# Performance work log

Measured on AMD Instinct MI355X. Metric: run time of the kernel, lower is better.

## Reference

```python
import jax, jax.numpy as jnp
import numpy as np
import math

B, C, H, W = 8, 96, 128, 128


def cos_map(N):
    wx = (jnp.arange(N, dtype=jnp.float32) + 0.5) / N          # [N]
    wn = jnp.arange(N, dtype=jnp.float32)[:, None]             # [N,1]
    w = jnp.cos(wn * wx[None, :] * jnp.pi) * math.sqrt(2.0 / N)
    return w.at[0, :].multiply(1.0 / math.sqrt(2.0))            # [N,N] (n, x)


def decay_map(h, w):
    wn = jnp.linspace(0.0, jnp.pi, h + 1)[:h][:, None]
    wm = jnp.linspace(0.0, jnp.pi, w + 1)[:w][None, :]
    return jnp.exp(-(wn ** 2 + wm ** 2))                        # [h,w]


def setup_inputs() -> dict:
    key = jax.random.key(0)
    ks = jax.random.split(key, 20)
    s = 0.02
    return {
        'x': jax.random.normal(ks[0], (B, C, H, W), jnp.float32),
        'freq_embed': jax.random.normal(ks[1], (H, W, C), jnp.float32),
        'outline_feat': jax.random.normal(ks[2], (B, H, W, C), jnp.float32),
        'dw_w': jax.random.normal(ks[3], (C, 1, 3, 3), jnp.float32) * s,
        'dw_b': jnp.zeros((C,), jnp.float32),
        'lin_w': jax.random.normal(ks[4], (2 * C, C), jnp.float32) * s,
        'lin_b': jnp.zeros((2 * C,), jnp.float32),
        'k_w': jax.random.normal(ks[5], (C, C), jnp.float32) * s,
        'k_b': jnp.zeros((C,), jnp.float32),
        'lin2_w': jax.random.normal(ks[6], (2 * C, 2 * C), jnp.float32) * s,
        'lin2_b': jnp.zeros((2 * C,), jnp.float32),
        'k2_w': jax.random.normal(ks[7], (2 * C, 2 * C), jnp.float32) * s,
        'k2_b': jnp.zeros((2 * C,), jnp.float32),
        'lin3_w': jax.random.normal(ks[8], (C, 2 * C), jnp.float32) * s,
        'lin3_b': jnp.zeros((C,), jnp.float32),
        'ln_g': jnp.ones((C,), jnp.float32),
        'ln_b': jnp.zeros((C,), jnp.float32),
        'out_w': jax.random.normal(ks[9], (C, C), jnp.float32) * s,
        'out_b': jnp.zeros((C,), jnp.float32),
    }


def dct2(u, cn, cm):
    # u: [B,H,W,C] -> [B,N,M,C]
    u = jnp.einsum('nh,bhwc->bnwc', cn, u)
    return jnp.einsum('mw,bnwc->bnmc', cm, u)


def idct2(u, cn, cm):
    # u: [B,N,M,C] -> [B,H,W,C]
    u = jnp.einsum('nh,bnmc->bhmc', cn, u)
    return jnp.einsum('mw,bhmc->bhwc', cm, u)


def layernorm(u, g, b, eps=1e-5):
    mu = jnp.mean(u, axis=-1, keepdims=True)
    var = jnp.var(u, axis=-1, keepdims=True)
    return (u - mu) * jax.lax.rsqrt(var + eps) * g + b


def reference(x, freq_embed, outline_feat, dw_w, dw_b, lin_w, lin_b, k_w, k_b,
              lin2_w, lin2_b, k2_w, k2_b, lin3_w, lin3_b, ln_g, ln_b, out_w, out_b):
    # depthwise 3x3 conv, padding 1 (NCHW)
    x = jax.lax.conv_general_dilated(
        x, dw_w, window_strides=(1, 1), padding=((1, 1), (1, 1)),
        dimension_numbers=('NCHW', 'OIHW', 'NCHW'), feature_group_count=C)
    x = x + dw_b[None, :, None, None]
    x = jnp.transpose(x, (0, 2, 3, 1))                          # [B,H,W,C]
    h = jnp.einsum('bhwc,dc->bhwd', x, lin_w) + lin_b           # [B,H,W,2C]
    x, z = jnp.split(h, 2, axis=-1)

    cn, cm = cos_map(H), cos_map(W)
    dec = decay_map(H, W)                                       # [H,W]

    # first heat pass
    x = dct2(x, cn, cm)                                         # [B,N,M,C]
    otfeat = jnp.mean(outline_feat, axis=0)                     # [H,W,C]
    k = jax.nn.relu(jnp.einsum('hwc,dc->hwd', freq_embed + otfeat, k_w) + k_b)
    x = x * jnp.power(dec[:, :, None], k)                       # [B,N,M,C]
    x = idct2(x, cn, cm)                                        # [B,H,W,C]

    # second heat pass on concatenated features
    x = jnp.concatenate([x, outline_feat], axis=-1)             # [B,H,W,2C]
    skfeat = jnp.mean(jnp.einsum('bhwc,dc->bhwd', x, lin2_w) + lin2_b, axis=0)  # [H,W,2C]
    x = dct2(x, cn, cm)
    k2 = jax.nn.relu(jnp.einsum('hwc,dc->hwd', skfeat, k2_w) + k2_b)
    x = x * jnp.power(dec[:, :, None], k2)
    x = idct2(x, cn, cm)                                        # [B,H,W,2C]

    x = jnp.einsum('bhwc,dc->bhwd', x, lin3_w) + lin3_b         # [B,H,W,C]
    x = layernorm(x, ln_g, ln_b)
    x = x * jax.nn.silu(z)
    x = jnp.einsum('bhwc,dc->bhwd', x, out_w) + out_b
    return jnp.transpose(x, (0, 3, 1, 2))                       # [B,C,H,W]
```

## Files before the change

### kernel.cpp

```cpp
#include <hip/hip_runtime.h>
#include <math.h>
#include <stdint.h>

#ifndef M_PI
#define M_PI 3.14159265358979323846
#endif

#define HW 16384
#define BHW 131072

typedef __attribute__((ext_vector_type(8))) short s8bf;
typedef __attribute__((ext_vector_type(4))) float f32x4;

union FragU { uint32_t u[4]; s8bf s; };

__device__ __forceinline__ uint32_t bf16h(float x) {
  uint32_t u = __float_as_uint(x);
  return (u + 0x7FFFu + ((u >> 16) & 1u)) >> 16;
}
__device__ __forceinline__ uint32_t packhl(float x) {
  uint32_t h = bf16h(x);
  float r = x - __uint_as_float(h << 16);
  return (h << 16) | bf16h(r);
}
__device__ __forceinline__ void unpack8(const uint32_t* w, s8bf& hi, s8bf& lo) {
  FragU H, L;
#pragma unroll
  for (int j = 0; j < 4; ++j) {
    H.u[j] = __builtin_amdgcn_perm(w[2 * j + 1], w[2 * j], 0x07060302u);
    L.u[j] = __builtin_amdgcn_perm(w[2 * j + 1], w[2 * j], 0x05040100u);
  }
  hi = H.s; lo = L.s;
}

__global__ void k0_tables(float* __restrict__ cc, float* __restrict__ ee) {
  int gid = blockIdx.x * 256 + threadIdx.x;
  int n = gid >> 7, m = gid & 127;
  double v = cos((double)n * ((double)m + 0.5) * (M_PI / 128.0)) * sqrt(2.0 / 128.0);
  if (n == 0) v *= 0.70710678118654752440;
  cc[gid] = (float)v;
  double wn = (double)n * (M_PI / 128.0), wm = (double)m * (M_PI / 128.0);
  ee[gid] = (float)(wn * wn + wm * wm);
}

__device__ __forceinline__ float cval(int a, int b) {
  double v = cos((double)a * ((double)b + 0.5) * (M_PI / 128.0)) * sqrt(2.0 / 128.0);
  if (a == 0) v *= 0.70710678118654752440;
  return (float)v;
}
__global__ void k0_frags(uint32_t* __restrict__ FAh, uint32_t* __restrict__ FAl,
                         uint32_t* __restrict__ FTh, uint32_t* __restrict__ FTl) {
  int tid = blockIdx.x * 256 + threadIdx.x;
  int lane = tid & 63, fid = tid >> 6;
  int mt = fid >> 2, ks = fid & 3;
  int n = 16 * mt + (lane & 15);
  int k0 = 32 * ks + 8 * (lane >> 4);
#pragma unroll
  for (int j = 0; j < 4; ++j) {
    float a0 = cval(n, k0 + 2 * j), a1 = cval(n, k0 + 2 * j + 1);
    uint32_t p0 = packhl(a0), p1 = packhl(a1);
    FAh[tid * 4 + j] = (p0 >> 16) | (p1 & 0xFFFF0000u);
    FAl[tid * 4 + j] = (p0 & 0xFFFFu) | (p1 << 16);
    float b0 = cval(k0 + 2 * j, n), b1 = cval(k0 + 2 * j + 1, n);
    uint32_t q0 = packhl(b0), q1 = packhl(b1);
    FTh[tid * 4 + j] = (q0 >> 16) | (q1 & 0xFFFF0000u);
    FTl[tid * 4 + j] = (q0 & 0xFFFFu) | (q1 << 16);
  }
}

__global__ void k_wfrag(const float* __restrict__ src, uint32_t* __restrict__ Fh,
                        uint32_t* __restrict__ Fl, int D, int K) {
  int tid = blockIdx.x * 256 + threadIdx.x;
  int nksl = K >> 5;
  int total = (D >> 4) * nksl * 64;
  if (tid >= total) return;
  int lane = tid & 63, fid = tid >> 6;
  int nt = fid / nksl, ksl = fid - nt * nksl;
  int d = 16 * nt + (lane & 15);
  int k0 = 32 * ksl + 8 * (lane >> 4);
#pragma unroll
  for (int j = 0; j < 4; ++j) {
    uint32_t p0 = packhl(src[d * K + k0 + 2 * j]);
    uint32_t p1 = packhl(src[d * K + k0 + 2 * j + 1]);
    Fh[tid * 4 + j] = (p0 >> 16) | (p1 & 0xFFFF0000u);
    Fl[tid * 4 + j] = (p0 & 0xFFFFu) | (p1 << 16);
  }
}

__global__ void k_wt(const float* __restrict__ src, float* __restrict__ dst, int D, int C) {
  int gid = blockIdx.x * 256 + threadIdx.x;
  if (gid >= D * C) return;
  int d = gid / C, c = gid % C;
  dst[c * D + d] = src[gid];
}

__global__ __launch_bounds__(256) void k_tfe(const float* __restrict__ fe,
                                             float* __restrict__ fet) {
  __shared__ float tile[64 * 97];
  int hw0 = blockIdx.x * 64;
  int tid = threadIdx.x;
#pragma unroll
  for (int t = 0; t < 24; ++t) {
    int l = tid + t * 256;
    int r = l / 96, c0 = l % 96;
    tile[r * 97 + c0] = fe[((size_t)hw0 + r) * 96 + c0];
  }
  __syncthreads();
#pragma unroll
  for (int t = 0; t < 24; ++t) {
    int l = tid + t * 256;
    int c0 = l >> 6, r = l & 63;
    fet[(size_t)c0 * HW + hw0 + r] = tile[r * 97 + c0];
  }
}

__global__ __launch_bounds__(256) void kconv(
    const float* __restrict__ x, const float* __restrict__ dw_w,
    const float* __restrict__ dw_b, float* __restrict__ xc) {
  int gid = blockIdx.x * 256 + threadIdx.x;
  int p = gid >> 12;
  int q = gid & 4095;
  int h = q >> 5, w4 = (q & 31) << 2;
  int c = p % 96;
  const float* pw = dw_w + c * 9;
  const float* row = x + (size_t)p * HW + h * 128 + w4;
  bool tp = h > 0, bt = h < 127, lf = w4 > 0, rt = w4 < 124;
  float4 t_, m_, b_;
  float tl, tr, ml, mr, bl, br;
  m_ = *(const float4*)row;
  ml = lf ? row[-1] : 0.f;
  mr = rt ? row[4] : 0.f;
  if (tp) {
    t_ = *(const float4*)(row - 128);
    tl = lf ? row[-129] : 0.f;
    tr = rt ? row[-124] : 0.f;
  } else { t_ = make_float4(0.f, 0.f, 0.f, 0.f); tl = tr = 0.f; }
  if (bt) {
    b_ = *(const float4*)(row + 128);
    bl = lf ? row[127] : 0.f;
    br = rt ? row[132] : 0.f;
  } else { b_ = make_float4(0.f, 0.f, 0.f, 0.f); bl = br = 0.f; }
  float w0 = pw[0], w1 = pw[1], w2 = pw[2], w3 = pw[3], w4w = pw[4],
        w5 = pw[5], w6 = pw[6], w7 = pw[7], w8 = pw[8];
  float bias = dw_b[c];
  float4 o;
  o.x = tl * w0 + t_.x * w1 + t_.y * w2 + ml * w3 + m_.x * w4w + m_.y * w5 + bl * w6 + b_.x * w7 + b_.y * w8 + bias;
  o.y = t_.x * w0 + t_.y * w1 + t_.z * w2 + m_.x * w3 + m_.y * w4w + m_.z * w5 + b_.x * w6 + b_.y * w7 + b_.z * w8 + bias;
  o.z = t_.y * w0 + t_.z * w1 + t_.w * w2 + m_.y * w3 + m_.z * w4w + m_.w * w5 + b_.y * w6 + b_.z * w7 + b_.w * w8 + bias;
  o.w = t_.z * w0 + t_.w * w1 + tr * w2 + m_.z * w3 + m_.w * w4w + mr * w5 + b_.z * w6 + b_.w * w7 + br * w8 + bias;
  *(float4*)(xc + (size_t)p * HW + h * 128 + w4) = o;
}

__global__ __launch_bounds__(256) void klin_mfma(
    const float* __restrict__ xc, const uint32_t* __restrict__ WLh,
    const uint32_t* __restrict__ WLl, const float* __restrict__ lin_b,
    float* __restrict__ x1p, float* __restrict__ z) {
  __shared__ uint32_t Ds[64 * 102];
  const int tid = threadIdx.x;
  const int lane = tid & 63;
  const int w = tid >> 6;
  const int l15 = lane & 15, lg = lane >> 4;
  const int gp0 = blockIdx.x * 64;
  const int b = gp0 >> 14, hw0 = gp0 & 16383;

#pragma unroll
  for (int i = 0; i < 24; ++i) {
    int k = w + 4 * i;
    float v = xc[((size_t)(b * 96 + k)) * HW + hw0 + lane];
    Ds[lane * 102 + k] = packhl(v);
  }
  __syncthreads();

  f32x4 acc[3][4];
#pragma unroll
  for (int nt = 0; nt < 3; ++nt) {
    float bv[4];
#pragma unroll
    for (int r = 0; r < 4; ++r) bv[r] = lin_b[16 * (3 * w + nt) + 4 * lg + r];
#pragma unroll
    for (int mt = 0; mt < 4; ++mt)
#pragma unroll
      for (int r = 0; r < 4; ++r) acc[nt][mt][r] = bv[r];
  }

#pragma unroll
  for (int ksl = 0; ksl < 3; ++ksl) {
    s8bf Dhi[4], Dlo[4];
#pragma unroll
    for (int mt = 0; mt < 4; ++mt) {
      const uint32_t* p = Ds + (16 * mt + l15) * 102 + 32 * ksl + 8 * lg;
      uint32_t wv[8];
      *(uint2*)&wv[0] = *(const uint2*)(p);
      *(uint2*)&wv[2] = *(const uint2*)(p + 2);
      *(uint2*)&wv[4] = *(const uint2*)(p + 4);
      *(uint2*)&wv[6] = *(const uint2*)(p + 6);
      unpack8(wv, Dhi[mt], Dlo[mt]);
    }
#pragma unroll
    for (int nt = 0; nt < 3; ++nt) {
      int base = (((3 * w + nt) * 3 + ksl) * 64 + lane) * 4;
      FragU H, L;
      *(uint4*)H.u = *(const uint4*)(WLh + base);
      *(uint4*)L.u = *(const uint4*)(WLl + base);
#pragma unroll
      for (int mt = 0; mt < 4; ++mt) {
        acc[nt][mt] = __builtin_amdgcn_mfma_f32_16x16x32_bf16(H.s, Dhi[mt], acc[nt][mt], 0, 0, 0);
        acc[nt][mt] = __builtin_amdgcn_mfma_f32_16x16x32_bf16(H.s, Dlo[mt], acc[nt][mt], 0, 0, 0);
        acc[nt][mt] = __builtin_amdgcn_mfma_f32_16x16x32_bf16(L.s, Dhi[mt], acc[nt][mt], 0, 0, 0);
      }
    }
  }
#pragma unroll
  for (int nt = 0; nt < 3; ++nt) {
    int d0 = 16 * (3 * w + nt) + 4 * lg;
#pragma unroll
    for (int mt = 0; mt < 4; ++mt) {
#pragma unroll
      for (int r = 0; r < 4; ++r) {
        int d = d0 + r;
        if (d < 96)
          x1p[((size_t)(b * 96 + d)) * HW + hw0 + 16 * mt + l15] = acc[nt][mt][r];
        else
          z[((size_t)(d - 96)) * BHW + gp0 + 16 * mt + l15] = acc[nt][mt][r];
      }
    }
  }
}

__global__ __launch_bounds__(256) void k3_transpose_mean(
    const float* __restrict__ of, float* __restrict__ ofp, float* __restrict__ cmU) {
  __shared__ float tile[64 * 97];
  int hw0 = blockIdx.x * 64;
  int tid = threadIdx.x;
  float sum[24];
#pragma unroll
  for (int t = 0; t < 24; ++t) sum[t] = 0.f;
  for (int b = 0; b < 8; ++b) {
    __syncthreads();
#pragma unroll
    for (int t = 0; t < 24; ++t) {
      int l = tid + t * 256;
      int r = l / 96, c0 = l % 96;
      tile[r * 97 + c0] = of[((size_t)b * 16384 + hw0 + r) * 96 + c0];
    }
    __syncthreads();
#pragma unroll
    for (int t = 0; t < 24; ++t) {
      int l = tid + t * 256;
      int c0 = l >> 6, r = l & 63;
      float v = tile[r * 97 + c0];
      sum[t] += v;
      ofp[(size_t)(b * 96 + c0) * HW + hw0 + r] = v;
    }
  }
#pragma unroll
  for (int t = 0; t < 24; ++t) {
    int l = tid + t * 256;
    int c0 = l >> 6, r = l & 63;
    cmU[(size_t)c0 * HW + hw0 + r] = sum[t] * 0.125f;
  }
}

__global__ __launch_bounds__(256) void k3b_kgemm(
    const float* __restrict__ fet, const float* __restrict__ otm,
    const float* __restrict__ kT, const float* __restrict__ kb,
    const float* __restrict__ ee, float* __restrict__ P1) {
  int tid = threadIdx.x;
  int lane = tid & 63;
  int n0 = __builtin_amdgcn_readfirstlane((tid >> 6) * 24);
  int row = blockIdx.x * 64 + lane;
  float acc[24];
#pragma unroll
  for (int j = 0; j < 24; ++j) acc[j] = kb[n0 + j];
#pragma unroll 4
  for (int c = 0; c < 96; ++c) {
    float a = fet[(size_t)c * HW + row] + otm[(size_t)c * HW + row];
    const float* wr = kT + c * 96 + n0;
#pragma unroll
    for (int j = 0; j < 24; ++j) acc[j] = fmaf(a, wr[j], acc[j]);
  }
  float er = ee[row];
#pragma unroll
  for (int j = 0; j < 24; ++j)
    P1[(size_t)(n0 + j) * HW + row] = expf(-er * fmaxf(acc[j], 0.f));
}

template <bool DATA_A>
__device__ __forceinline__ void heat_step(
    const uint32_t* __restrict__ Fh, const uint32_t* __restrict__ Fl,
    const uint32_t* __restrict__ Ds, f32x4 (&acc)[4][4], int wm, int wn, int lane) {
  const int l15 = lane & 15, lg = lane >> 4;
  const int wd = DATA_A ? wm : wn;
  const int wf = DATA_A ? wn : wm;
#pragma unroll
  for (int ksl = 0; ksl < 4; ++ksl) {
    s8bf Dhi[4], Dlo[4], Fhi[4], Flo[4];
#pragma unroll
    for (int t = 0; t < 4; ++t) {
      const uint32_t* p = Ds + (64 * wd + 16 * t + l15) * 130 + 32 * ksl + 8 * lg;
      uint32_t wv[8];
      *(uint2*)&wv[0] = *(const uint2*)(p);
      *(uint2*)&wv[2] = *(const uint2*)(p + 2);
      *(uint2*)&wv[4] = *(const uint2*)(p + 4);
      *(uint2*)&wv[6] = *(const uint2*)(p + 6);
      unpack8(wv, Dhi[t], Dlo[t]);
    }
#pragma unroll
    for (int t = 0; t < 4; ++t) {
      int base = (((4 * wf + t) * 4 + ksl) * 64 + lane) * 4;
      FragU H, L;
      *(uint4*)H.u = *(const uint4*)(Fh + base);
      *(uint4*)L.u = *(const uint4*)(Fl + base);
      Fhi[t] = H.s; Flo[t] = L.s;
    }
    const s8bf* Ah = DATA_A ? Dhi : Fhi;
    const s8bf* Al = DATA_A ? Dlo : Flo;
    const s8bf* Bh = DATA_A ? Fhi : Dhi;
    const s8bf* Bl = DATA_A ? Flo : Dlo;
#pragma unroll
    for (int mi = 0; mi < 4; ++mi)
#pragma unroll
      for (int ni = 0; ni < 4; ++ni)
        acc[mi][ni] = __builtin_amdgcn_mfma_f32_16x16x32_bf16(Ah[mi], Bh[ni], acc[mi][ni], 0, 0, 0);
#pragma unroll
    for (int mi = 0; mi < 4; ++mi)
#pragma unroll
      for (int ni = 0; ni < 4; ++ni)
        acc[mi][ni] = __builtin_amdgcn_mfma_f32_16x16x32_bf16(Ah[mi], Bl[ni], acc[mi][ni], 0, 0, 0);
#pragma unroll
    for (int mi = 0; mi < 4; ++mi)
#pragma unroll
      for (int ni = 0; ni < 4; ++ni)
        acc[mi][ni] = __builtin_amdgcn_mfma_f32_16x16x32_bf16(Al[mi], Bh[ni], acc[mi][ni], 0, 0, 0);
  }
}

template <bool USE_P>
__global__ __launch_bounds__(256, 2) void heat_half(
    const float* __restrict__ In, float* __restrict__ Out,
    const float* __restrict__ P, const uint32_t* __restrict__ Fh,
    const uint32_t* __restrict__ Fl, int Cmod) {
  __shared__ uint32_t Ds[128 * 130];
  const int tid = threadIdx.x;
  const int lane = tid & 63;
  const int w = tid >> 6;
  const int wm = w >> 1, wn = w & 1;
  const int l15 = lane & 15, lg = lane >> 4;
  const float* Ip = In + (size_t)blockIdx.x * HW;
  float* Op = Out + (size_t)blockIdx.x * HW;
  const float* Pp = nullptr;
  if constexpr (USE_P) Pp = P + (size_t)(blockIdx.x % Cmod) * HW;

  {
    int col = tid & 127, r0 = tid >> 7;
#pragma unroll
    for (int i = 0; i < 64; ++i) {
      int row = r0 + 2 * i;
      Ds[col * 130 + row] = packhl(Ip[row * 128 + col]);
    }
  }
  __syncthreads();

  f32x4 acc[4][4];
  const f32x4 zero4 = {0.f, 0.f, 0.f, 0.f};
#pragma unroll
  for (int mi = 0; mi < 4; ++mi)
#pragma unroll
    for (int ni = 0; ni < 4; ++ni) acc[mi][ni] = zero4;
  heat_step<false>(Fh, Fl, Ds, acc, wm, wn, lane);
  __syncthreads();
#pragma unroll
  for (int mi = 0; mi < 4; ++mi)
#pragma unroll
    for (int ni = 0; ni < 4; ++ni)
#pragma unroll
      for (int r = 0; r < 4; ++r)
        Ds[(64 * wm + 16 * mi + 4 * lg + r) * 130 + 64 * wn + 16 * ni + l15] =
            packhl(acc[mi][ni][r]);
  __syncthreads();

#pragma unroll
  for (int mi = 0; mi < 4; ++mi)
#pragma unroll
    for (int ni = 0; ni < 4; ++ni) acc[mi][ni] = zero4;
  heat_step<true>(Fh, Fl, Ds, acc, wm, wn, lane);
#pragma unroll
  for (int mi = 0; mi < 4; ++mi)
#pragma unroll
    for (int ni = 0; ni < 4; ++ni) {
      int row = 64 * wm + 16 * mi + 4 * lg;
      int col = 64 * wn + 16 * ni + l15;
#pragma unroll
      for (int r = 0; r < 4; ++r) {
        float v = acc[mi][ni][r];
        if constexpr (USE_P) v *= Pp[(row + r) * 128 + col];
        Op[(row + r) * 128 + col] = v;
      }
    }
}

__global__ void k5_mean(const float* __restrict__ src, float* __restrict__ dst) {
  int idx = blockIdx.x * 256 + threadIdx.x;
  int c = idx >> 14, s = idx & 16383;
  float sum = 0.f;
#pragma unroll
  for (int b = 0; b < 8; ++b) sum += src[(size_t)(b * 96 + c) * HW + s];
  dst[idx] = sum * 0.125f;
}

__global__ __launch_bounds__(256) void k67_mfma(
    const float* __restrict__ cm,
    const uint32_t* __restrict__ W2h, const uint32_t* __restrict__ W2l,
    const float* __restrict__ b2,
    const uint32_t* __restrict__ K2h, const uint32_t* __restrict__ K2l,
    const float* __restrict__ b2k, const float* __restrict__ ee,
    float* __restrict__ P2) {
  __shared__ uint32_t Ds[64 * 194];
  const int tid = threadIdx.x;
  const int lane = tid & 63;
  const int w = tid >> 6;
  const int l15 = lane & 15, lg = lane >> 4;
  const int row0 = blockIdx.x * 64;

#pragma unroll
  for (int i = 0; i < 48; ++i) {
    int k = w + 4 * i;
    Ds[lane * 194 + k] = packhl(cm[(size_t)k * HW + row0 + lane]);
  }
  __syncthreads();

  f32x4 acc[3][4];
#pragma unroll
  for (int nt = 0; nt < 3; ++nt) {
    float bv[4];
#pragma unroll
    for (int r = 0; r < 4; ++r) bv[r] = b2[16 * (3 * w + nt) + 4 * lg + r];
#pragma unroll
    for (int mt = 0; mt < 4; ++mt)
#pragma unroll
      for (int r = 0; r < 4; ++r) acc[nt][mt][r] = bv[r];
  }
#pragma unroll
  for (int ksl = 0; ksl < 6; ++ksl) {
    s8bf Dhi[4], Dlo[4];
#pragma unroll
    for (int mt = 0; mt < 4; ++mt) {
      const uint32_t* p = Ds + (16 * mt + l15) * 194 + 32 * ksl + 8 * lg;
      uint32_t wv[8];
      *(uint2*)&wv[0] = *(const uint2*)(p);
      *(uint2*)&wv[2] = *(const uint2*)(p + 2);
      *(uint2*)&wv[4] = *(const uint2*)(p + 4);
      *(uint2*)&wv[6] = *(const uint2*)(p + 6);
      unpack8(wv, Dhi[mt], Dlo[mt]);
    }
#pragma unroll
    for (int nt = 0; nt < 3; ++nt) {
      int base = (((3 * w + nt) * 6 + ksl) * 64 + lane) * 4;
      FragU H, L;
      *(uint4*)H.u = *(const uint4*)(W2h + base);
      *(uint4*)L.u = *(const uint4*)(W2l + base);
#pragma unroll
      for (int mt = 0; mt < 4; ++mt) {
        acc[nt][mt] = __builtin_amdgcn_mfma_f32_16x16x32_bf16(H.s, Dhi[mt], acc[nt][mt], 0, 0, 0);
        acc[nt][mt] = __builtin_amdgcn_mfma_f32_16x16x32_bf16(H.s, Dlo[mt], acc[nt][mt], 0, 0, 0);
        acc[nt][mt] = __builtin_amdgcn_mfma_f32_16x16x32_bf16(L.s, Dhi[mt], acc[nt][mt], 0, 0, 0);
      }
    }
  }
  __syncthreads();
#pragma unroll
  for (int nt = 0; nt < 3; ++nt) {
    int d0 = 16 * (3 * w + nt) + 4 * lg;
#pragma unroll
    for (int mt = 0; mt < 4; ++mt) {
      int col = 16 * mt + l15;
#pragma unroll
      for (int r = 0; r < 4; ++r)
        Ds[col * 194 + d0 + r] = packhl(acc[nt][mt][r]);
    }
  }
  __syncthreads();

  f32x4 acc2[3][4];
#pragma unroll
  for (int nt = 0; nt < 3; ++nt) {
    float bv[4];
#pragma unroll
    for (int r = 0; r < 4; ++r) bv[r] = b2k[16 * (3 * w + nt) + 4 * lg + r];
#pragma unroll
    for (int mt = 0; mt < 4; ++mt)
#pragma unroll
      for (int r = 0; r < 4; ++r) acc2[nt][mt][r] = bv[r];
  }
#pragma unroll
  for (int ksl = 0; ksl < 6; ++ksl) {
    s8bf Dhi[4], Dlo[4];
#pragma unroll
    for (int mt = 0; mt < 4; ++mt) {
      const uint32_t* p = Ds + (16 * mt + l15) * 194 + 32 * ksl + 8 * lg;
      uint32_t wv[8];
      *(uint2*)&wv[0] = *(const uint2*)(p);
      *(uint2*)&wv[2] = *(const uint2*)(p + 2);
      *(uint2*)&wv[4] = *(const uint2*)(p + 4);
      *(uint2*)&wv[6] = *(const uint2*)(p + 6);
      unpack8(wv, Dhi[mt], Dlo[mt]);
    }
#pragma unroll
    for (int nt = 0; nt < 3; ++nt) {
      int base = (((3 * w + nt) * 6 + ksl) * 64 + lane) * 4;
      FragU H, L;
      *(uint4*)H.u = *(const uint4*)(K2h + base);
      *(uint4*)L.u = *(const uint4*)(K2l + base);
#pragma unroll
      for (int mt = 0; mt < 4; ++mt) {
        acc2[nt][mt] = __builtin_amdgcn_mfma_f32_16x16x32_bf16(H.s, Dhi[mt], acc2[nt][mt], 0, 0, 0);
        acc2[nt][mt] = __builtin_amdgcn_mfma_f32_16x16x32_bf16(H.s, Dlo[mt], acc2[nt][mt], 0, 0, 0);
        acc2[nt][mt] = __builtin_amdgcn_mfma_f32_16x16x32_bf16(L.s, Dhi[mt], acc2[nt][mt], 0, 0, 0);
      }
    }
  }
  float er[4];
#pragma unroll
  for (int mt = 0; mt < 4; ++mt) er[mt] = ee[row0 + 16 * mt + l15];
#pragma unroll
  for (int nt = 0; nt < 3; ++nt) {
    int d0 = 16 * (3 * w + nt) + 4 * lg;
#pragma unroll
    for (int mt = 0; mt < 4; ++mt) {
      int row = row0 + 16 * mt + l15;
#pragma unroll
      for (int r = 0; r < 4; ++r)
        P2[(size_t)(d0 + r) * HW + row] = expf(-er[mt] * fmaxf(acc2[nt][mt][r], 0.f));
    }
  }
}

__global__ __launch_bounds__(256) void kmix(
    const float* __restrict__ S1, const float* __restrict__ OhP,
    const float* __restrict__ P2,
    const uint32_t* __restrict__ W3h, const uint32_t* __restrict__ W3l,
    float* __restrict__ Tf) {
  __shared__ uint32_t Ds[128 * 98];
  const int tid = threadIdx.x;
  const int lane = tid & 63;
  const int w = tid >> 6;
  const int wn = w >> 1, wm = w & 1;
  const int l15 = lane & 15, lg = lane >> 4;
  const int gp0 = blockIdx.x * 128;
  const int b = gp0 >> 14, hw0 = gp0 & 16383;

  f32x4 acc[3][4];
#pragma unroll
  for (int i = 0; i < 3; ++i)
#pragma unroll
    for (int j = 0; j < 4; ++j)
#pragma unroll
      for (int r = 0; r < 4; ++r) acc[i][j][r] = 0.f;

#pragma unroll
  for (int c = 0; c < 2; ++c) {
    if (c) __syncthreads();
#pragma unroll
    for (int i = 0; i < 24; ++i) {
      int k = w + 4 * i;
      if (c == 0) {
        const float* sp = S1 + ((size_t)(b * 96 + k)) * HW + hw0;
        const float* pp = P2 + (size_t)k * HW + hw0;
        Ds[lane * 98 + k] = packhl(sp[lane] * pp[lane]);
        Ds[(lane + 64) * 98 + k] = packhl(sp[lane + 64] * pp[lane + 64]);
      } else {
        const float* sp = OhP + ((size_t)(b * 96 + k)) * HW + hw0;
        Ds[lane * 98 + k] = packhl(sp[lane]);
        Ds[(lane + 64) * 98 + k] = packhl(sp[lane + 64]);
      }
    }
    __syncthreads();
#pragma unroll
    for (int ksl = 0; ksl < 3; ++ksl) {
      s8bf Dhi[4], Dlo[4];
#pragma unroll
      for (int j = 0; j < 4; ++j) {
        const uint32_t* p = Ds + (16 * (4 * wm + j) + l15) * 98 + 32 * ksl + 8 * lg;
        uint32_t wv[8];
        *(uint2*)&wv[0] = *(const uint2*)(p);
        *(uint2*)&wv[2] = *(const uint2*)(p + 2);
        *(uint2*)&wv[4] = *(const uint2*)(p + 4);
        *(uint2*)&wv[6] = *(const uint2*)(p + 6);
        unpack8(wv, Dhi[j], Dlo[j]);
      }
#pragma unroll
      for (int i = 0; i < 3; ++i) {
        int base = (((3 * wn + i) * 6 + 3 * c + ksl) * 64 + lane) * 4;
        FragU H, L;
        *(uint4*)H.u = *(const uint4*)(W3h + base);
        *(uint4*)L.u = *(const uint4*)(W3l + base);
#pragma unroll
        for (int j = 0; j < 4; ++j) {
          acc[i][j] = __builtin_amdgcn_mfma_f32_16x16x32_bf16(H.s, Dhi[j], acc[i][j], 0, 0, 0);
          acc[i][j] = __builtin_amdgcn_mfma_f32_16x16x32_bf16(H.s, Dlo[j], acc[i][j], 0, 0, 0);
          acc[i][j] = __builtin_amdgcn_mfma_f32_16x16x32_bf16(L.s, Dhi[j], acc[i][j], 0, 0, 0);
        }
      }
    }
  }
#pragma unroll
  for (int i = 0; i < 3; ++i) {
    int d0 = 16 * (3 * wn + i) + 4 * lg;
#pragma unroll
    for (int j = 0; j < 4; ++j) {
      int hw = hw0 + 16 * (4 * wm + j) + l15;
#pragma unroll
      for (int r = 0; r < 4; ++r)
        Tf[((size_t)(b * 96 + d0 + r)) * HW + hw] = acc[i][j][r];
    }
  }
}

__global__ __launch_bounds__(256) void k9r(
    const float* __restrict__ y3, const float* __restrict__ z,
    const float* __restrict__ lin3b,
    const float* __restrict__ lng, const float* __restrict__ lnb,
    const uint32_t* __restrict__ WOh, const uint32_t* __restrict__ WOl,
    const float* __restrict__ outb, float* __restrict__ out) {
  __shared__ uint32_t Ds2[128 * 98];
  __shared__ float2 red[4][128];
  const int tid = threadIdx.x;
  const int lane = tid & 63;
  const int w = tid >> 6;
  const int wn = w >> 1, wm = w & 1;
  const int l15 = lane & 15, lg = lane >> 4;
  const int gp0 = blockIdx.x * 128;
  const int b = gp0 >> 14, hw0 = gp0 & 16383;

  float vA[24], vB[24];
  float sA = 0.f, qA = 0.f, sB = 0.f, qB = 0.f;
#pragma unroll
  for (int i = 0; i < 24; ++i) {
    int k = w + 4 * i;
    const float* yp = y3 + ((size_t)(b * 96 + k)) * HW + hw0;
    float bk = lin3b[k];
    float tA = yp[lane] + bk;      vA[i] = tA; sA += tA; qA = fmaf(tA, tA, qA);
    float tB = yp[lane + 64] + bk; vB[i] = tB; sB += tB; qB = fmaf(tB, tB, qB);
  }
  red[w][lane] = make_float2(sA, qA);
  red[w][lane + 64] = make_float2(sB, qB);
  __syncthreads();
  float2 a0 = red[0][lane], a1 = red[1][lane], a2 = red[2][lane], a3 = red[3][lane];
  float2 b0 = red[0][lane + 64], b1 = red[1][lane + 64], b2_ = red[2][lane + 64], b3 = red[3][lane + 64];
  float muA = (a0.x + a1.x + a2.x + a3.x) * (1.f / 96.f);
  float vrA = (a0.y + a1.y + a2.y + a3.y) * (1.f / 96.f) - muA * muA;
  float invA = rsqrtf(fmaxf(vrA, 0.f) + 1e-5f);
  float muB = (b0.x + b1.x + b2_.x + b3.x) * (1.f / 96.f);
  float vrB = (b0.y + b1.y + b2_.y + b3.y) * (1.f / 96.f) - muB * muB;
  float invB = rsqrtf(fmaxf(vrB, 0.f) + 1e-5f);
#pragma unroll
  for (int i = 0; i < 24; ++i) {
    int k = w + 4 * i;
    const float* zp = z + (size_t)k * BHW + gp0;
    float g = lng[k], bb = lnb[k];
    float zA = zp[lane];
    float uA = (vA[i] - muA) * invA * g + bb;
    Ds2[lane * 98 + k] = packhl(uA * (zA / (1.f + expf(-zA))));
    float zB = zp[lane + 64];
    float uB = (vB[i] - muB) * invB * g + bb;
    Ds2[(lane + 64) * 98 + k] = packhl(uB * (zB / (1.f + expf(-zB))));
  }
  __syncthreads();

  f32x4 acc2[3][4];
#pragma unroll
  for (int i = 0; i < 3; ++i) {
    float bv[4];
#pragma unroll
    for (int r = 0; r < 4; ++r) bv[r] = outb[16 * (3 * wn + i) + 4 * lg + r];
#pragma unroll
    for (int j = 0; j < 4; ++j)
#pragma unroll
      for (int r = 0; r < 4; ++r) acc2[i][j][r] = bv[r];
  }
#pragma unroll
  for (int ksl = 0; ksl < 3; ++ksl) {
    s8bf Dhi[4], Dlo[4];
#pragma unroll
    for (int j = 0; j < 4; ++j) {
      const uint32_t* p = Ds2 + (16 * (4 * wm + j) + l15) * 98 + 32 * ksl + 8 * lg;
      uint32_t wv[8];
      *(uint2*)&wv[0] = *(const uint2*)(p);
      *(uint2*)&wv[2] = *(const uint2*)(p + 2);
      *(uint2*)&wv[4] = *(const uint2*)(p + 4);
      *(uint2*)&wv[6] = *(const uint2*)(p + 6);
      unpack8(wv, Dhi[j], Dlo[j]);
    }
#pragma unroll
    for (int i = 0; i < 3; ++i) {
      int base = (((3 * wn + i) * 3 + ksl) * 64 + lane) * 4;
      FragU H, L;
      *(uint4*)H.u = *(const uint4*)(WOh + base);
      *(uint4*)L.u = *(const uint4*)(WOl + base);
#pragma unroll
      for (int j = 0; j < 4; ++j) {
        acc2[i][j] = __builtin_amdgcn_mfma_f32_16x16x32_bf16(H.s, Dhi[j], acc2[i][j], 0, 0, 0);
        acc2[i][j] = __builtin_amdgcn_mfma_f32_16x16x32_bf16(H.s, Dlo[j], acc2[i][j], 0, 0, 0);
        acc2[i][j] = __builtin_amdgcn_mfma_f32_16x16x32_bf16(L.s, Dhi[j], acc2[i][j], 0, 0, 0);
      }
    }
  }
#pragma unroll
  for (int i = 0; i < 3; ++i) {
    int d0 = 16 * (3 * wn + i) + 4 * lg;
#pragma unroll
    for (int j = 0; j < 4; ++j) {
      int hw = hw0 + 16 * (4 * wm + j) + l15;
#pragma unroll
      for (int r = 0; r < 4; ++r)
        out[((size_t)(b * 96 + d0 + r)) * HW + hw] = acc2[i][j][r];
    }
  }
}

extern "C" void kernel_launch(void* const* d_in, const int* in_sizes, int n_in,
                              void* d_out, int out_size, void* d_ws, size_t ws_size,
                              hipStream_t stream) {
  const float* x      = (const float*)d_in[0];
  const float* fe     = (const float*)d_in[1];
  const float* of     = (const float*)d_in[2];
  const float* dw_w   = (const float*)d_in[3];
  const float* dw_b   = (const float*)d_in[4];
  const float* lin_w  = (const float*)d_in[5];
  const float* lin_b  = (const float*)d_in[6];
  const float* k_w    = (const float*)d_in[7];
  const float* k_b    = (const float*)d_in[8];
  const float* lin2_w = (const float*)d_in[9];
  const float* lin2_b = (const float*)d_in[10];
  const float* k2_w   = (const float*)d_in[11];
  const float* k2_b   = (const float*)d_in[12];
  const float* lin3_w = (const float*)d_in[13];
  const float* lin3_b = (const float*)d_in[14];
  const float* ln_g   = (const float*)d_in[15];
  const float* ln_b   = (const float*)d_in[16];
  const float* out_w  = (const float*)d_in[17];
  const float* out_b  = (const float*)d_in[18];
  float* out = (float*)d_out;

  float* ws    = (float*)d_ws;
  float* x1p   = ws;
  float* z     = x1p   + 12582912;
  float* ofp   = z     + 12582912;
  float* cm    = ofp   + 12582912;
  float* skf   = cm    + 3145728;
  float* P1    = skf   + 3145728;
  float* P2    = P1    + 1572864;
  float* cc    = P2    + 3145728;
  float* ee    = cc    + 16384;
  float* linT  = ee    + 16384;
  float* kT    = linT  + 18432;
  float* lin2T = kT    + 9216;
  float* k2T   = lin2T + 36864;
  float* lin3T = k2T   + 36864;
  float* outT  = lin3T + 18432;
  float* fet   = outT  + 9216;
  uint32_t* FAh = (uint32_t*)(fet + 1572864);
  uint32_t* FAl = FAh + 8192;
  uint32_t* FTh = FAl + 8192;
  uint32_t* FTl = FTh + 8192;
  uint32_t* WLh = FTl + 8192;
  uint32_t* WLl = WLh + 9216;
  uint32_t* W3h = WLl + 9216;
  uint32_t* W3l = W3h + 9216;
  uint32_t* WOh = W3l + 9216;
  uint32_t* WOl = WOh + 4608;
  uint32_t* W2h = WOl + 4608;
  uint32_t* W2l = W2h + 18432;
  uint32_t* K2h = W2l + 18432;
  uint32_t* K2l = K2h + 18432;
  float* xc    = ofp;
  float* cmSf  = skf;
  (void)in_sizes; (void)n_in; (void)out_size; (void)ws_size;

  k0_tables<<<64, 256, 0, stream>>>(cc, ee);
  k0_frags<<<8, 256, 0, stream>>>(FAh, FAl, FTh, FTl);
  k_wfrag<<<9, 256, 0, stream>>>(lin_w, WLh, WLl, 192, 96);
  k_wfrag<<<9, 256, 0, stream>>>(lin3_w, W3h, W3l, 96, 192);
  k_wfrag<<<5, 256, 0, stream>>>(out_w, WOh, WOl, 96, 96);
  k_wfrag<<<18, 256, 0, stream>>>(lin2_w, W2h, W2l, 192, 192);
  k_wfrag<<<18, 256, 0, stream>>>(k2_w, K2h, K2l, 192, 192);
  k_wt<<<36, 256, 0, stream>>>(k_w, kT, 96, 96);
  k_tfe<<<256, 256, 0, stream>>>(fe, fet);

  kconv<<<12288, 256, 0, stream>>>(x, dw_w, dw_b, xc);
  klin_mfma<<<2048, 256, 0, stream>>>(xc, WLh, WLl, lin_b, x1p, z);
  k3_transpose_mean<<<256, 256, 0, stream>>>(of, ofp, cm + (size_t)96 * HW);
  k3b_kgemm<<<256, 256, 0, stream>>>(fet, cm + (size_t)96 * HW, kT, k_b, ee, P1);
  heat_half<true><<<768, 256, 0, stream>>>(x1p, x1p, P1, FAh, FAl, 96);
  k5_mean<<<6144, 256, 0, stream>>>(x1p, cmSf);
  heat_half<false><<<96, 256, 0, stream>>>(cmSf, cm, nullptr, FTh, FTl, 96);
  k67_mfma<<<256, 256, 0, stream>>>(cm, W2h, W2l, lin2_b, K2h, K2l, k2_b, ee, P2);
  heat_half<true><<<768, 256, 0, stream>>>(ofp, ofp, P2 + (size_t)96 * HW, FAh, FAl, 96);
  kmix<<<1024, 256, 0, stream>>>(x1p, ofp, P2, W3h, W3l, x1p);
  heat_half<false><<<768, 256, 0, stream>>>(x1p, x1p, nullptr, FTh, FTl, 96);
  k9r<<<1024, 256, 0, stream>>>(x1p, z, lin3_b, ln_g, ln_b, WOh, WOl, out_b, out);
}
```

Before: 377.7 us.

## Merge prep kernels, store intermediates pre-split bf16 hi/lo, prefetch z in k9r

```diff
diff --git a/kernel.cpp b/kernel.cpp
--- a/kernel.cpp
+++ b/kernel.cpp
@@ -33,44 +33,16 @@
   hi = H.s; lo = L.s;
 }
 
-__global__ void k0_tables(float* __restrict__ cc, float* __restrict__ ee) {
-  int gid = blockIdx.x * 256 + threadIdx.x;
-  int n = gid >> 7, m = gid & 127;
-  double v = cos((double)n * ((double)m + 0.5) * (M_PI / 128.0)) * sqrt(2.0 / 128.0);
-  if (n == 0) v *= 0.70710678118654752440;
-  cc[gid] = (float)v;
-  double wn = (double)n * (M_PI / 128.0), wm = (double)m * (M_PI / 128.0);
-  ee[gid] = (float)(wn * wn + wm * wm);
-}
-
 __device__ __forceinline__ float cval(int a, int b) {
   double v = cos((double)a * ((double)b + 0.5) * (M_PI / 128.0)) * sqrt(2.0 / 128.0);
   if (a == 0) v *= 0.70710678118654752440;
   return (float)v;
 }
-__global__ void k0_frags(uint32_t* __restrict__ FAh, uint32_t* __restrict__ FAl,
-                         uint32_t* __restrict__ FTh, uint32_t* __restrict__ FTl) {
-  int tid = blockIdx.x * 256 + threadIdx.x;
-  int lane = tid & 63, fid = tid >> 6;
-  int mt = fid >> 2, ks = fid & 3;
-  int n = 16 * mt + (lane & 15);
-  int k0 = 32 * ks + 8 * (lane >> 4);
-#pragma unroll
-  for (int j = 0; j < 4; ++j) {
-    float a0 = cval(n, k0 + 2 * j), a1 = cval(n, k0 + 2 * j + 1);
-    uint32_t p0 = packhl(a0), p1 = packhl(a1);
-    FAh[tid * 4 + j] = (p0 >> 16) | (p1 & 0xFFFF0000u);
-    FAl[tid * 4 + j] = (p0 & 0xFFFFu) | (p1 << 16);
-    float b0 = cval(k0 + 2 * j, n), b1 = cval(k0 + 2 * j + 1, n);
-    uint32_t q0 = packhl(b0), q1 = packhl(b1);
-    FTh[tid * 4 + j] = (q0 >> 16) | (q1 & 0xFFFF0000u);
-    FTl[tid * 4 + j] = (q0 & 0xFFFFu) | (q1 << 16);
-  }
-}
-
-__global__ void k_wfrag(const float* __restrict__ src, uint32_t* __restrict__ Fh,
-                        uint32_t* __restrict__ Fl, int D, int K) {
-  int tid = blockIdx.x * 256 + threadIdx.x;
+
+__device__ __forceinline__ void wfrag_dev(const float* __restrict__ src,
+                                          uint32_t* __restrict__ Fh,
+                                          uint32_t* __restrict__ Fl,
+                                          int D, int K, int tid) {
   int nksl = K >> 5;
   int total = (D >> 4) * nksl * 64;
   if (tid >= total) return;
@@ -87,30 +59,71 @@
   }
 }
 
-__global__ void k_wt(const float* __restrict__ src, float* __restrict__ dst, int D, int C) {
-  int gid = blockIdx.x * 256 + threadIdx.x;
-  if (gid >= D * C) return;
-  int d = gid / C, c = gid % C;
-  dst[c * D + d] = src[gid];
-}
-
-__global__ __launch_bounds__(256) void k_tfe(const float* __restrict__ fe,
-                                             float* __restrict__ fet) {
+__global__ __launch_bounds__(256) void kprep(
+    float* __restrict__ ee,
+    uint32_t* __restrict__ FAh, uint32_t* __restrict__ FAl,
+    uint32_t* __restrict__ FTh, uint32_t* __restrict__ FTl,
+    const float* __restrict__ lin_w, uint32_t* __restrict__ WLh, uint32_t* __restrict__ WLl,
+    const float* __restrict__ lin3_w, uint32_t* __restrict__ W3h, uint32_t* __restrict__ W3l,
+    const float* __restrict__ out_w, uint32_t* __restrict__ WOh, uint32_t* __restrict__ WOl,
+    const float* __restrict__ lin2_w, uint32_t* __restrict__ W2h, uint32_t* __restrict__ W2l,
+    const float* __restrict__ k2_w, uint32_t* __restrict__ K2h, uint32_t* __restrict__ K2l,
+    const float* __restrict__ k_w, float* __restrict__ kT,
+    const float* __restrict__ fe, float* __restrict__ fet) {
   __shared__ float tile[64 * 97];
-  int hw0 = blockIdx.x * 64;
-  int tid = threadIdx.x;
-#pragma unroll
-  for (int t = 0; t < 24; ++t) {
-    int l = tid + t * 256;
-    int r = l / 96, c0 = l % 96;
-    tile[r * 97 + c0] = fe[((size_t)hw0 + r) * 96 + c0];
-  }
-  __syncthreads();
-#pragma unroll
-  for (int t = 0; t < 24; ++t) {
-    int l = tid + t * 256;
-    int c0 = l >> 6, r = l & 63;
-    fet[(size_t)c0 * HW + hw0 + r] = tile[r * 97 + c0];
+  const int bb = blockIdx.x;
+  const int tid = threadIdx.x;
+  if (bb < 64) {
+    int gid = bb * 256 + tid;
+    int n = gid >> 7, m = gid & 127;
+    double wn = (double)n * (M_PI / 128.0), wm = (double)m * (M_PI / 128.0);
+    ee[gid] = (float)(wn * wn + wm * wm);
+  } else if (bb < 72) {
+    int t2 = (bb - 64) * 256 + tid;
+    int lane = t2 & 63, fid = t2 >> 6;
+    int mt = fid >> 2, ks = fid & 3;
+    int n = 16 * mt + (lane & 15);
+    int k0 = 32 * ks + 8 * (lane >> 4);
+#pragma unroll
+    for (int j = 0; j < 4; ++j) {
+      uint32_t p0 = packhl(cval(n, k0 + 2 * j)), p1 = packhl(cval(n, k0 + 2 * j + 1));
+      FAh[t2 * 4 + j] = (p0 >> 16) | (p1 & 0xFFFF0000u);
+      FAl[t2 * 4 + j] = (p0 & 0xFFFFu) | (p1 << 16);
+      uint32_t q0 = packhl(cval(k0 + 2 * j, n)), q1 = packhl(cval(k0 + 2 * j + 1, n));
+      FTh[t2 * 4 + j] = (q0 >> 16) | (q1 & 0xFFFF0000u);
+      FTl[t2 * 4 + j] = (q0 & 0xFFFFu) | (q1 << 16);
+    }
+  } else if (bb < 81) {
+    wfrag_dev(lin_w, WLh, WLl, 192, 96, (bb - 72) * 256 + tid);
+  } else if (bb < 90) {
+    wfrag_dev(lin3_w, W3h, W3l, 96, 192, (bb - 81) * 256 + tid);
+  } else if (bb < 95) {
+    wfrag_dev(out_w, WOh, WOl, 96, 96, (bb - 90) * 256 + tid);
+  } else if (bb < 113) {
+    wfrag_dev(lin2_w, W2h, W2l, 192, 192, (bb - 95) * 256 + tid);
+  } else if (bb < 131) {
+    wfrag_dev(k2_w, K2h, K2l, 192, 192, (bb - 113) * 256 + tid);
+  } else if (bb < 167) {
+    int gid = (bb - 131) * 256 + tid;
+    if (gid < 96 * 96) {
+      int d = gid / 96, c = gid % 96;
+      kT[c * 96 + d] = k_w[gid];
+    }
+  } else {
+    int hw0 = (bb - 167) * 64;
+#pragma unroll
+    for (int t = 0; t < 24; ++t) {
+      int l = tid + t * 256;
+      int r = l / 96, c0 = l % 96;
+      tile[r * 97 + c0] = fe[((size_t)hw0 + r) * 96 + c0];
+    }
+    __syncthreads();
+#pragma unroll
+    for (int t = 0; t < 24; ++t) {
+      int l = tid + t * 256;
+      int c0 = l >> 6, r = l & 63;
+      fet[(size_t)c0 * HW + hw0 + r] = tile[r * 97 + c0];
+    }
   }
 }
 
@@ -154,7 +167,7 @@
 __global__ __launch_bounds__(256) void klin_mfma(
     const float* __restrict__ xc, const uint32_t* __restrict__ WLh,
     const uint32_t* __restrict__ WLl, const float* __restrict__ lin_b,
-    float* __restrict__ x1p, float* __restrict__ z) {
+    uint32_t* __restrict__ x1u, float* __restrict__ z) {
   __shared__ uint32_t Ds[64 * 102];
   const int tid = threadIdx.x;
   const int lane = tid & 63;
@@ -219,7 +232,7 @@
       for (int r = 0; r < 4; ++r) {
         int d = d0 + r;
         if (d < 96)
-          x1p[((size_t)(b * 96 + d)) * HW + hw0 + 16 * mt + l15] = acc[nt][mt][r];
+          x1u[((size_t)(b * 96 + d)) * HW + hw0 + 16 * mt + l15] = packhl(acc[nt][mt][r]);
         else
           z[((size_t)(d - 96)) * BHW + gp0 + 16 * mt + l15] = acc[nt][mt][r];
       }
@@ -228,7 +241,7 @@
 }
 
 __global__ __launch_bounds__(256) void k3_transpose_mean(
-    const float* __restrict__ of, float* __restrict__ ofp, float* __restrict__ cmU) {
+    const float* __restrict__ of, uint32_t* __restrict__ ofu, float* __restrict__ cmU) {
   __shared__ float tile[64 * 97];
   int hw0 = blockIdx.x * 64;
   int tid = threadIdx.x;
@@ -250,7 +263,7 @@
       int c0 = l >> 6, r = l & 63;
       float v = tile[r * 97 + c0];
       sum[t] += v;
-      ofp[(size_t)(b * 96 + c0) * HW + hw0 + r] = v;
+      ofu[(size_t)(b * 96 + c0) * HW + hw0 + r] = packhl(v);
     }
   }
 #pragma unroll
@@ -335,7 +348,7 @@
   }
 }
 
-template <bool USE_P>
+template <bool PIN, bool POUT, bool USE_P>
 __global__ __launch_bounds__(256, 2) void heat_half(
     const float* __restrict__ In, float* __restrict__ Out,
     const float* __restrict__ P, const uint32_t* __restrict__ Fh,
@@ -353,10 +366,19 @@
 
   {
     int col = tid & 127, r0 = tid >> 7;
-#pragma unroll
-    for (int i = 0; i < 64; ++i) {
-      int row = r0 + 2 * i;
-      Ds[col * 130 + row] = packhl(Ip[row * 128 + col]);
+    if constexpr (PIN) {
+      const uint32_t* Iu = (const uint32_t*)Ip;
+#pragma unroll
+      for (int i = 0; i < 64; ++i) {
+        int row = r0 + 2 * i;
+        Ds[col * 130 + row] = Iu[row * 128 + col];
+      }
+    } else {
+#pragma unroll
+      for (int i = 0; i < 64; ++i) {
+        int row = r0 + 2 * i;
+        Ds[col * 130 + row] = packhl(Ip[row * 128 + col]);
+      }
     }
   }
   __syncthreads();
@@ -394,7 +416,10 @@
       for (int r = 0; r < 4; ++r) {
         float v = acc[mi][ni][r];
         if constexpr (USE_P) v *= Pp[(row + r) * 128 + col];
-        Op[(row + r) * 128 + col] = v;
+        if constexpr (POUT)
+          ((uint32_t*)Op)[(row + r) * 128 + col] = packhl(v);
+        else
+          Op[(row + r) * 128 + col] = v;
       }
     }
 }
@@ -536,10 +561,10 @@
 }
 
 __global__ __launch_bounds__(256) void kmix(
-    const float* __restrict__ S1, const float* __restrict__ OhP,
+    const float* __restrict__ S1, const uint32_t* __restrict__ OhU,
     const float* __restrict__ P2,
     const uint32_t* __restrict__ W3h, const uint32_t* __restrict__ W3l,
-    float* __restrict__ Tf) {
+    uint32_t* __restrict__ TfU) {
   __shared__ uint32_t Ds[128 * 98];
   const int tid = threadIdx.x;
   const int lane = tid & 63;
@@ -569,9 +594,9 @@
         Ds[lane * 98 + k] = packhl(sp[lane] * pp[lane]);
         Ds[(lane + 64) * 98 + k] = packhl(sp[lane + 64] * pp[lane + 64]);
       } else {
-        const float* sp = OhP + ((size_t)(b * 96 + k)) * HW + hw0;
-        Ds[lane * 98 + k] = packhl(sp[lane]);
-        Ds[(lane + 64) * 98 + k] = packhl(sp[lane + 64]);
+        const uint32_t* sp = OhU + ((size_t)(b * 96 + k)) * HW + hw0;
+        Ds[lane * 98 + k] = sp[lane];
+        Ds[(lane + 64) * 98 + k] = sp[lane + 64];
       }
     }
     __syncthreads();
@@ -611,7 +636,7 @@
       int hw = hw0 + 16 * (4 * wm + j) + l15;
 #pragma unroll
       for (int r = 0; r < 4; ++r)
-        Tf[((size_t)(b * 96 + d0 + r)) * HW + hw] = acc[i][j][r];
+        TfU[((size_t)(b * 96 + d0 + r)) * HW + hw] = packhl(acc[i][j][r]);
     }
   }
 }
@@ -622,7 +647,7 @@
     const float* __restrict__ lng, const float* __restrict__ lnb,
     const uint32_t* __restrict__ WOh, const uint32_t* __restrict__ WOl,
     const float* __restrict__ outb, float* __restrict__ out) {
-  __shared__ uint32_t Ds2[128 * 98];
+  __shared__ uint32_t Ds2[128 * 97];
   __shared__ float2 red[4][128];
   const int tid = threadIdx.x;
   const int lane = tid & 63;
@@ -632,6 +657,14 @@
   const int gp0 = blockIdx.x * 128;
   const int b = gp0 >> 14, hw0 = gp0 & 16383;
 
+  float zA[24], zB[24];
+#pragma unroll
+  for (int i = 0; i < 24; ++i) {
+    int k = w + 4 * i;
+    const float* zp = z + (size_t)k * BHW + gp0;
+    zA[i] = zp[lane];
+    zB[i] = zp[lane + 64];
+  }
   float vA[24], vB[24];
   float sA = 0.f, qA = 0.f, sB = 0.f, qB = 0.f;
 #pragma unroll
@@ -656,14 +689,11 @@
 #pragma unroll
   for (int i = 0; i < 24; ++i) {
     int k = w + 4 * i;
-    const float* zp = z + (size_t)k * BHW + gp0;
     float g = lng[k], bb = lnb[k];
-    float zA = zp[lane];
     float uA = (vA[i] - muA) * invA * g + bb;
-    Ds2[lane * 98 + k] = packhl(uA * (zA / (1.f + expf(-zA))));
-    float zB = zp[lane + 64];
+    Ds2[lane * 97 + k] = packhl(uA * (zA[i] / (1.f + __expf(-zA[i]))));
     float uB = (vB[i] - muB) * invB * g + bb;
-    Ds2[(lane + 64) * 98 + k] = packhl(uB * (zB / (1.f + expf(-zB))));
+    Ds2[(lane + 64) * 97 + k] = packhl(uB * (zB[i] / (1.f + __expf(-zB[i]))));
   }
   __syncthreads();
 
@@ -683,7 +713,7 @@
     s8bf Dhi[4], Dlo[4];
 #pragma unroll
     for (int j = 0; j < 4; ++j) {
-      const uint32_t* p = Ds2 + (16 * (4 * wm + j) + l15) * 98 + 32 * ksl + 8 * lg;
+      const uint32_t* p = Ds2 + (16 * (4 * wm + j) + l15) * 97 + 32 * ksl + 8 * lg;
       uint32_t wv[8];
       *(uint2*)&wv[0] = *(const uint2*)(p);
       *(uint2*)&wv[2] = *(const uint2*)(p + 2);
@@ -775,28 +805,25 @@
   uint32_t* K2l = K2h + 18432;
   float* xc    = ofp;
   float* cmSf  = skf;
+  uint32_t* x1u = (uint32_t*)x1p;
+  uint32_t* ofu = (uint32_t*)ofp;
   (void)in_sizes; (void)n_in; (void)out_size; (void)ws_size;
 
-  k0_tables<<<64, 256, 0, stream>>>(cc, ee);
-  k0_frags<<<8, 256, 0, stream>>>(FAh, FAl, FTh, FTl);
-  k_wfrag<<<9, 256, 0, stream>>>(lin_w, WLh, WLl, 192, 96);
-  k_wfrag<<<9, 256, 0, stream>>>(lin3_w, W3h, W3l, 96, 192);
-  k_wfrag<<<5, 256, 0, stream>>>(out_w, WOh, WOl, 96, 96);
-  k_wfrag<<<18, 256, 0, stream>>>(lin2_w, W2h, W2l, 192, 192);
-  k_wfrag<<<18, 256, 0, stream>>>(k2_w, K2h, K2l, 192, 192);
-  k_wt<<<36, 256, 0, stream>>>(k_w, kT, 96, 96);
-  k_tfe<<<256, 256, 0, stream>>>(fe, fet);
+  kprep<<<423, 256, 0, stream>>>(ee, FAh, FAl, FTh, FTl,
+                                 lin_w, WLh, WLl, lin3_w, W3h, W3l,
+                                 out_w, WOh, WOl, lin2_w, W2h, W2l,
+                                 k2_w, K2h, K2l, k_w, kT, fe, fet);
 
   kconv<<<12288, 256, 0, stream>>>(x, dw_w, dw_b, xc);
-  klin_mfma<<<2048, 256, 0, stream>>>(xc, WLh, WLl, lin_b, x1p, z);
-  k3_transpose_mean<<<256, 256, 0, stream>>>(of, ofp, cm + (size_t)96 * HW);
+  klin_mfma<<<2048, 256, 0, stream>>>(xc, WLh, WLl, lin_b, x1u, z);
+  k3_transpose_mean<<<256, 256, 0, stream>>>(of, ofu, cm + (size_t)96 * HW);
   k3b_kgemm<<<256, 256, 0, stream>>>(fet, cm + (size_t)96 * HW, kT, k_b, ee, P1);
-  heat_half<true><<<768, 256, 0, stream>>>(x1p, x1p, P1, FAh, FAl, 96);
+  heat_half<true, false, true><<<768, 256, 0, stream>>>(x1p, x1p, P1, FAh, FAl, 96);
   k5_mean<<<6144, 256, 0, stream>>>(x1p, cmSf);
-  heat_half<false><<<96, 256, 0, stream>>>(cmSf, cm, nullptr, FTh, FTl, 96);
+  heat_half<false, false, false><<<96, 256, 0, stream>>>(cmSf, cm, nullptr, FTh, FTl, 96);
   k67_mfma<<<256, 256, 0, stream>>>(cm, W2h, W2l, lin2_b, K2h, K2l, k2_b, ee, P2);
-  heat_half<true><<<768, 256, 0, stream>>>(ofp, ofp, P2 + (size_t)96 * HW, FAh, FAl, 96);
-  kmix<<<1024, 256, 0, stream>>>(x1p, ofp, P2, W3h, W3l, x1p);
-  heat_half<false><<<768, 256, 0, stream>>>(x1p, x1p, nullptr, FTh, FTl, 96);
+  heat_half<true, true, true><<<768, 256, 0, stream>>>(ofp, ofp, P2 + (size_t)96 * HW, FAh, FAl, 96);
+  kmix<<<1024, 256, 0, stream>>>(x1p, ofu, P2, W3h, W3l, x1u);
+  heat_half<true, false, false><<<768, 256, 0, stream>>>(x1p, x1p, nullptr, FTh, FTl, 96);
   k9r<<<1024, 256, 0, stream>>>(x1p, z, lin3_b, ln_g, ln_b, WOh, WOl, out_b, out);
 }
```

Measured after the change: 358.5 us. 1.05x faster.
